# Kernel tuning notes

Hardware: AMD Instinct MI355X
Metric: run time of the kernel (lower is better)

Reference implementation:

```python
import jax, jax.numpy as jnp
import numpy as np

N_NODES = 10000
N_EDGES = 80000
N_GRAPHS = 64
HEADS = 8
F_IN = 128
D1, D2, D3 = 512, 256, 128  # per-head (and output, concat=False) widths
OUT_DIM = 10


def _lin(key, fin, fout):
    kw, kb = jax.random.split(key)
    w = jax.random.normal(kw, (fin, fout), dtype=jnp.float32) * 0.05
    b = jax.random.normal(kb, (fout,), dtype=jnp.float32) * 0.05
    return w, b


def setup_inputs() -> dict:
    key = jax.random.key(0)
    ks = jax.random.split(key, 24)
    x = jax.random.normal(ks[0], (N_NODES, F_IN), dtype=jnp.float32)
    edge_index = jax.random.randint(ks[1], (2, N_EDGES), 0, N_NODES, dtype=jnp.int64)
    batch = jnp.sort(jax.random.randint(ks[2], (N_NODES,), 0, N_GRAPHS, dtype=jnp.int64))
    d = {"x": x, "edge_index": edge_index, "batch": batch}
    # conv1: 128 -> heads*512 (q,k,v), skip 128 -> 512
    d["w_q1"], d["b_q1"] = _lin(ks[3], F_IN, HEADS * D1)
    d["w_k1"], d["b_k1"] = _lin(ks[4], F_IN, HEADS * D1)
    d["w_v1"], d["b_v1"] = _lin(ks[5], F_IN, HEADS * D1)
    d["w_s1"], d["b_s1"] = _lin(ks[6], F_IN, D1)
    # conv2: 512 -> heads*256, skip 512 -> 256
    d["w_q2"], d["b_q2"] = _lin(ks[7], D1, HEADS * D2)
    d["w_k2"], d["b_k2"] = _lin(ks[8], D1, HEADS * D2)
    d["w_v2"], d["b_v2"] = _lin(ks[9], D1, HEADS * D2)
    d["w_s2"], d["b_s2"] = _lin(ks[10], D1, D2)
    # conv3: 256 -> heads*128, skip 256 -> 128
    d["w_q3"], d["b_q3"] = _lin(ks[11], D2, HEADS * D3)
    d["w_k3"], d["b_k3"] = _lin(ks[12], D2, HEADS * D3)
    d["w_v3"], d["b_v3"] = _lin(ks[13], D2, HEADS * D3)
    d["w_s3"], d["b_s3"] = _lin(ks[14], D2, D3)
    # global attention gate + final fc
    d["w_g"], d["b_g"] = _lin(ks[15], D3, 1)
    d["w_fc"], d["b_fc"] = _lin(ks[16], D3, OUT_DIM)
    return d


def _seg_softmax(a, seg, n):
    m = jax.ops.segment_max(a, seg, num_segments=n)
    e = jnp.exp(a - m[seg])
    s = jax.ops.segment_sum(e, seg, num_segments=n)
    return e / (s[seg] + 1e-16)


def _tconv(x, edge_index, wq, bq, wk, bk, wv, bv, ws, bs):
    # PyG TransformerConv, concat=False, root_weight=True, no edge features
    n = x.shape[0]
    c = wq.shape[1] // HEADS
    q = (x @ wq + bq).reshape(n, HEADS, c)
    k = (x @ wk + bk).reshape(n, HEADS, c)
    v = (x @ wv + bv).reshape(n, HEADS, c)
    src, dst = edge_index[0], edge_index[1]
    a = jnp.einsum('ehc,ehc->eh', q[dst], k[src]) / jnp.sqrt(jnp.float32(c))
    alpha = _seg_softmax(a, dst, n)                                  # [E, H]
    out = jax.ops.segment_sum(v[src] * alpha[..., None], dst, num_segments=n)
    return out.mean(axis=1) + (x @ ws + bs)                          # mean over heads + skip


def reference(x, edge_index, batch,
              w_q1, b_q1, w_k1, b_k1, w_v1, b_v1, w_s1, b_s1,
              w_q2, b_q2, w_k2, b_k2, w_v2, b_v2, w_s2, b_s2,
              w_q3, b_q3, w_k3, b_k3, w_v3, b_v3, w_s3, b_s3,
              w_g, b_g, w_fc, b_fc):
    h = jax.nn.elu(_tconv(x, edge_index, w_q1, b_q1, w_k1, b_k1, w_v1, b_v1, w_s1, b_s1))
    h = jax.nn.elu(_tconv(h, edge_index, w_q2, b_q2, w_k2, b_k2, w_v2, b_v2, w_s2, b_s2))
    h = jax.nn.elu(_tconv(h, edge_index, w_q3, b_q3, w_k3, b_k3, w_v3, b_v3, w_s3, b_s3))
    # GlobalAttention pooling: softmax(gate) over nodes within each graph
    gate = h @ w_g + b_g                                             # [N, 1]
    gate = _seg_softmax(gate, batch, N_GRAPHS)
    g = jax.ops.segment_sum(gate * h, batch, num_segments=N_GRAPHS)  # [G, D3]
    return g @ w_fc + b_fc                                           # [G, OUT_DIM]
```

## Files before the change

kernel.cpp:

```cpp
#include <hip/hip_runtime.h>
#include <math.h>

typedef __bf16 bf16;
typedef __bf16 bf16x8 __attribute__((ext_vector_type(8)));
typedef __bf16 bf16x4 __attribute__((ext_vector_type(4)));
typedef __bf16 bf16x2 __attribute__((ext_vector_type(2)));
typedef float f32x4 __attribute__((ext_vector_type(4)));
typedef float f32x2 __attribute__((ext_vector_type(2)));
typedef unsigned int u32;

#define N_NODES 10000
#define N_EDGES 80000
#define N_GRAPHS 64

template<int EPL> struct VecT;
template<> struct VecT<8>{ typedef bf16x8 type; };
template<> struct VecT<4>{ typedef bf16x4 type; };
template<> struct VecT<2>{ typedef bf16x2 type; };

__device__ inline void gload_lds16(const bf16* g, bf16* l){
  __builtin_amdgcn_global_load_lds(
      (const __attribute__((address_space(1))) unsigned int*)g,
      (__attribute__((address_space(3))) unsigned int*)l, 16, 0, 0);
}

__global__ __launch_bounds__(256) void detect_f32_k(const unsigned short* __restrict__ raw, int n,
                                                    int* __restrict__ flagF){
  int i = blockIdx.x*256 + threadIdx.x;
  if (i < n){
    unsigned e = (raw[i] >> 7) & 0xFFu;
    if (e >= 0xC0u) atomicOr(flagF, 1);
  }
}

struct CvPack {
  const void* src[11];
  bf16* dst[11];
  int pre[12];
  int rl[11];
  int st[11];
};
__global__ __launch_bounds__(256) void convert_all(CvPack p, const int* __restrict__ flagF){
  int gid = blockIdx.x*256 + threadIdx.x;
  if (gid >= p.pre[11]) return;
  int t = 0;
  while (gid >= p.pre[t+1]) ++t;
  int i = gid - p.pre[t];
  bool f = (*flagF != 0);
  float v = f ? ((const float*)p.src[t])[i] : (float)((const bf16*)p.src[t])[i];
  int row = i / p.rl[t], col = i - row*p.rl[t];
  p.dst[t][(size_t)row*p.st[t] + col] = (bf16)v;
}

__global__ __launch_bounds__(256) void detect_i64(const int* __restrict__ raw, int* __restrict__ flag){
  int i = blockIdx.x*256 + threadIdx.x;
  if (i < 4000 && raw[2*i+1] != 0) atomicOr(flag, 1);
}

__global__ __launch_bounds__(256) void conv_idx(const int* __restrict__ ei_raw,
                                                const int* __restrict__ b_raw,
                                                const int* __restrict__ flag,
                                                int* __restrict__ src, int* __restrict__ dst,
                                                int* __restrict__ bat, int* __restrict__ cnt){
  int i = blockIdx.x*256 + threadIdx.x;
  bool i32 = (*flag != 0);
  if (i < N_EDGES){
    int s = i32 ? ei_raw[i]   : ei_raw[2*i];
    int d = i32 ? ei_raw[N_EDGES + i] : ei_raw[2*(N_EDGES + i)];
    s = min(max(s, 0), N_NODES-1);
    d = min(max(d, 0), N_NODES-1);
    src[i] = s; dst[i] = d;
    atomicAdd(&cnt[d], 1);
  }
  if (i < N_NODES){
    int b = i32 ? b_raw[i] : b_raw[2*i];
    bat[i] = min(max(b, 0), N_GRAPHS-1);
  }
}

__global__ __launch_bounds__(256) void scanA(const int* __restrict__ cnt, int* __restrict__ fill,
                                             int* __restrict__ bsum, int N){
  __shared__ int s[256];
  int i = blockIdx.x*256 + threadIdx.x;
  int v = (i < N) ? cnt[i] : 0;
  s[threadIdx.x] = v;
  __syncthreads();
  for (int d = 1; d < 256; d <<= 1){
    int t = (threadIdx.x >= d) ? s[threadIdx.x - d] : 0;
    __syncthreads();
    s[threadIdx.x] += t;
    __syncthreads();
  }
  if (i < N) fill[i] = s[threadIdx.x] - v;
  if (threadIdx.x == 255) bsum[blockIdx.x] = s[255];
}
__global__ __launch_bounds__(64) void scanB(int* __restrict__ bsum, int nb){
  if (threadIdx.x == 0){
    int a = 0;
    for (int b = 0; b < nb; ++b){ int t = bsum[b]; bsum[b] = a; a += t; }
  }
}
__global__ __launch_bounds__(256) void scanC(const int* __restrict__ bsum, int* __restrict__ fill,
                                             int* __restrict__ row_ptr, int N){
  int i = blockIdx.x*256 + threadIdx.x;
  if (i < N){
    int st = fill[i] + bsum[i >> 8];
    fill[i] = st;
    row_ptr[i] = st;
  }
  if (i == 0) row_ptr[N] = N_EDGES;
}

__global__ __launch_bounds__(256) void fill_csr(const int* __restrict__ dst,
                                                int* __restrict__ fill, int* __restrict__ eids){
  int e = blockIdx.x*256 + threadIdx.x;
  if (e < N_EDGES){
    int p = atomicAdd(&fill[dst[e]], 1);
    eids[p] = e;
  }
}

__global__ __launch_bounds__(256)
void gemm_bias(const bf16* __restrict__ A, int lda,
               const bf16* __restrict__ Bt,
               const bf16* __restrict__ bias, bf16* __restrict__ Cout, int ldc,
               int M, int N, int K)
{
  __shared__ bf16 As[128*64];
  __shared__ bf16 Bs[128*64];
  const int tid = threadIdx.x;
  const int lane = tid & 63;
  const int wave = tid >> 6;
  const int m0 = blockIdx.y * 128, n0 = blockIdx.x * 128;
  const int wm = (wave >> 1) * 64, wn = (wave & 1) * 64;
  const int l15 = lane & 15, l4 = lane >> 4;
  const int srow = lane >> 3;
  const int schunk = lane & 7;

  f32x4 acc[4][4] = {};

  for (int k0 = 0; k0 < K; k0 += 64){
    #pragma unroll
    for (int j = 0; j < 4; ++j){
      int r0 = (wave*4 + j)*8;
      int r  = r0 + srow;
      int gc = schunk ^ (r & 7);
      int ga = m0 + r; if (ga >= M) ga = M-1;
      gload_lds16(A  + (size_t)ga*lda      + k0 + gc*8, As + r0*64);
      gload_lds16(Bt + (size_t)(n0 + r)*K  + k0 + gc*8, Bs + r0*64);
    }
    __syncthreads();
    #pragma unroll
    for (int kt = 0; kt < 2; ++kt){
      bf16x8 af[4], bfr[4];
      #pragma unroll
      for (int mt = 0; mt < 4; ++mt){
        int row = wm + mt*16 + l15;
        int p = (kt*4 + l4) ^ (l15 & 7);
        af[mt] = *(const bf16x8*)(As + row*64 + p*8);
      }
      #pragma unroll
      for (int nt = 0; nt < 4; ++nt){
        int row = wn + nt*16 + l15;
        int p = (kt*4 + l4) ^ (l15 & 7);
        bfr[nt] = *(const bf16x8*)(Bs + row*64 + p*8);
      }
      #pragma unroll
      for (int mt = 0; mt < 4; ++mt)
        #pragma unroll
        for (int nt = 0; nt < 4; ++nt)
          acc[mt][nt] = __builtin_amdgcn_mfma_f32_16x16x32_bf16(af[mt], bfr[nt], acc[mt][nt], 0, 0, 0);
    }
    __syncthreads();
  }

  #pragma unroll
  for (int nt = 0; nt < 4; ++nt){
    int col = n0 + wn + nt*16 + l15;
    float bv = (float)bias[col];
    #pragma unroll
    for (int mt = 0; mt < 4; ++mt){
      int rbase = m0 + wm + mt*16 + l4*4;
      #pragma unroll
      for (int r = 0; r < 4; ++r){
        int row = rbase + r;
        if (row < M) Cout[(size_t)row*ldc + col] = (bf16)(acc[mt][nt][r] + bv);
      }
    }
  }
}

template<int NKB>
__global__ __launch_bounds__(512, 1)
void gemm_bres_bias(const bf16* __restrict__ A, int lda,
                    const bf16* __restrict__ Bt,
                    const bf16* __restrict__ bias, bf16* __restrict__ Cout, int ldc,
                    int M, int YB)
{
  constexpr int K = NKB*64;
  __shared__ bf16 Bs[NKB][128*64];
  const int tid = threadIdx.x;
  const int lane = tid & 63;
  const int wave = tid >> 6;
  const int n0 = blockIdx.x * 128;
  const int l15 = lane & 15, l4 = lane >> 4;
  const int srow = lane >> 3;
  const int schunk = lane & 7;

  #pragma unroll
  for (int kb = 0; kb < NKB; ++kb){
    #pragma unroll
    for (int j = 0; j < 2; ++j){
      int r0 = (wave*2 + j)*8;
      int r  = r0 + srow;
      int gc = schunk ^ srow;
      gload_lds16(Bt + (size_t)(n0 + r)*K + kb*64 + gc*8, &Bs[kb][r0*64]);
    }
  }
  asm volatile("s_waitcnt vmcnt(0)" ::: "memory");
  __builtin_amdgcn_s_barrier();

  float bv[8];
  #pragma unroll
  for (int nt = 0; nt < 8; ++nt) bv[nt] = (float)bias[n0 + nt*16 + l15];

  const int nstrips = (M + 63) >> 6;
  const int ws0 = blockIdx.y*8 + wave;
  const int wstep = YB*8;

  for (int strip = ws0; strip < nstrips; strip += wstep){
    const int m0 = strip*64;
    f32x4 acc[4][8] = {};
    #pragma unroll 2
    for (int kk = 0; kk < K/32; ++kk){
      const int kb = kk >> 1, kt = kk & 1;
      bf16x8 af[4];
      #pragma unroll
      for (int mt = 0; mt < 4; ++mt){
        int row = m0 + mt*16 + l15; if (row >= M) row = M-1;
        af[mt] = *(const bf16x8*)(A + (size_t)row*lda + kk*32 + l4*8);
      }
      bf16x8 bfr[8];
      #pragma unroll
      for (int nt = 0; nt < 8; ++nt){
        int p = (kt*4 + l4) ^ (l15 & 7);
        bfr[nt] = *(const bf16x8*)(&Bs[kb][(nt*16 + l15)*64 + p*8]);
      }
      #pragma unroll
      for (int mt = 0; mt < 4; ++mt)
        #pragma unroll
        for (int nt = 0; nt < 8; ++nt)
          acc[mt][nt] = __builtin_amdgcn_mfma_f32_16x16x32_bf16(af[mt], bfr[nt], acc[mt][nt], 0, 0, 0);
    }
    #pragma unroll
    for (int mt = 0; mt < 4; ++mt){
      int rbase = m0 + mt*16 + l4*4;
      #pragma unroll
      for (int r = 0; r < 4; ++r){
        int row = rbase + r;
        if (row < M){
          #pragma unroll
          for (int nt = 0; nt < 8; ++nt)
            Cout[(size_t)row*ldc + n0 + nt*16 + l15] = (bf16)(acc[mt][nt][r] + bv[nt]);
        }
      }
    }
  }
}

__global__ __launch_bounds__(512, 1)
void gemm8p_bias(const bf16* __restrict__ A, int lda,
                 const bf16* __restrict__ Bt,
                 const bf16* __restrict__ bias, bf16* __restrict__ Cout, int ldc,
                 int M, int K)
{
  __shared__ bf16 As[3][256*64];
  __shared__ bf16 Bs[3][128*64];
  const int tid = threadIdx.x;
  const int lane = tid & 63;
  const int wave = tid >> 6;
  const int m0 = blockIdx.y * 256, n0 = blockIdx.x * 128;
  const int wm = (wave >> 1) * 64;
  const int wn = (wave & 1) * 64;
  const int l15 = lane & 15, l4 = lane >> 4;
  const int srow = lane >> 3;
  const int schunk = lane & 7;
  const int NT = K >> 6;

  auto stageA = [&](int t, int j){
    int b = t % 3;
    int r0 = (wave + j*8)*8;
    int r  = r0 + srow;
    int gc = schunk ^ srow;
    int ga = m0 + r; if (ga >= M) ga = M-1;
    gload_lds16(A + (size_t)ga*lda + t*64 + gc*8, &As[b][r0*64]);
  };
  auto stageB = [&](int t, int j){
    int b = t % 3;
    int r0 = (wave + j*8)*8;
    int r  = r0 + srow;
    int gc = schunk ^ srow;
    gload_lds16(Bt + (size_t)(n0 + r)*K + t*64 + gc*8, &Bs[b][r0*64]);
  };

  stageA(0,0); stageA(0,1); stageA(0,2); stageA(0,3); stageB(0,0); stageB(0,1);
  if (NT > 1){ stageA(1,0); stageA(1,1); stageA(1,2); stageA(1,3); stageB(1,0); stageB(1,1); }
  if (NT > 1) asm volatile("s_waitcnt vmcnt(6)" ::: "memory");
  else        asm volatile("s_waitcnt vmcnt(0)" ::: "memory");
  __builtin_amdgcn_s_barrier();

  f32x4 acc[4][4] = {};

  for (int t = 0; t < NT; ++t){
    const bf16* as = &As[t % 3][0];
    const bf16* bs = &Bs[t % 3][0];
    bf16x8 bfr[4][2];
    bf16x8 af[2][2];

    #pragma unroll
    for (int nt2 = 0; nt2 < 4; ++nt2)
      #pragma unroll
      for (int kt = 0; kt < 2; ++kt){
        int row = wn + nt2*16 + l15;
        int p = (kt*4 + l4) ^ (l15 & 7);
        bfr[nt2][kt] = *(const bf16x8*)(bs + row*64 + p*8);
      }
    #pragma unroll
    for (int i = 0; i < 2; ++i)
      #pragma unroll
      for (int kt = 0; kt < 2; ++kt){
        int row = wm + i*16 + l15;
        int p = (kt*4 + l4) ^ (l15 & 7);
        af[i][kt] = *(const bf16x8*)(as + row*64 + p*8);
      }
    if (t + 2 < NT){ stageA(t+2,0); stageA(t+2,1); stageB(t+2,0); }
    __builtin_amdgcn_s_setprio(1);
    #pragma unroll
    for (int i = 0; i < 2; ++i)
      #pragma unroll
      for (int nt2 = 0; nt2 < 4; ++nt2)
        #pragma unroll
        for (int kt = 0; kt < 2; ++kt)
          acc[i][nt2] = __builtin_amdgcn_mfma_f32_16x16x32_bf16(af[i][kt], bfr[nt2][kt], acc[i][nt2], 0, 0, 0);
    __builtin_amdgcn_s_setprio(0);

    #pragma unroll
    for (int i = 0; i < 2; ++i)
      #pragma unroll
      for (int kt = 0; kt < 2; ++kt){
        int row = wm + (2+i)*16 + l15;
        int p = (kt*4 + l4) ^ (l15 & 7);
        af[i][kt] = *(const bf16x8*)(as + row*64 + p*8);
      }
    if (t + 2 < NT){ stageA(t+2,2); stageA(t+2,3); stageB(t+2,1); }
    __builtin_amdgcn_s_setprio(1);
    #pragma unroll
    for (int i = 0; i < 2; ++i)
      #pragma unroll
      for (int nt2 = 0; nt2 < 4; ++nt2)
        #pragma unroll
        for (int kt = 0; kt < 2; ++kt)
          acc[2+i][nt2] = __builtin_amdgcn_mfma_f32_16x16x32_bf16(af[i][kt], bfr[nt2][kt], acc[2+i][nt2], 0, 0, 0);
    __builtin_amdgcn_s_setprio(0);

    if (t < NT - 1){
      if (t + 2 < NT) asm volatile("s_waitcnt vmcnt(6)" ::: "memory");
      else            asm volatile("s_waitcnt vmcnt(0)" ::: "memory");
      __builtin_amdgcn_s_barrier();
    }
  }

  #pragma unroll
  for (int nt2 = 0; nt2 < 4; ++nt2){
    int col = n0 + wn + nt2*16 + l15;
    float bv = (float)bias[col];
    #pragma unroll
    for (int mt = 0; mt < 4; ++mt){
      int rbase = m0 + wm + mt*16 + l4*4;
      #pragma unroll
      for (int r = 0; r < 4; ++r){
        int row = rbase + r;
        if (row < M) Cout[(size_t)row*ldc + col] = (bf16)(acc[mt][nt2][r] + bv);
      }
    }
  }
}

template<int BM, int OUTMODE>
__global__ __launch_bounds__(256)
void gemm_fused(const bf16* __restrict__ A, int lda,
                const bf16* __restrict__ Bt,
                const bf16* __restrict__ bp, const bf16* __restrict__ mb,
                const int* __restrict__ row_ptr,
                bf16* __restrict__ outB, int ldo, float* __restrict__ outF,
                int M, int K)
{
  constexpr int PA    = BM/32;
  constexpr int WCOLS = 128/BM;
  constexpr int WTN   = BM;
  constexpr int NT    = WTN/16;
  __shared__ bf16 As[BM*64];
  __shared__ bf16 Bs[128*64];
  const int tid = threadIdx.x;
  const int lane = tid & 63;
  const int wave = tid >> 6;
  const int m0 = blockIdx.y * BM, n0 = blockIdx.x * 128;
  const int wm = (wave / WCOLS) * 32;
  const int wn = (wave % WCOLS) * WTN;
  const int l15 = lane & 15, l4 = lane >> 4;
  const int srow = lane >> 3;
  const int schunk = lane & 7;

  f32x4 acc[2][NT] = {};

  for (int k0 = 0; k0 < K; k0 += 64){
    #pragma unroll
    for (int j = 0; j < PA; ++j){
      int r0 = (wave*PA + j)*8;
      int r  = r0 + srow;
      int gc = schunk ^ (r & 7);
      int ga = m0 + r; if (ga >= M) ga = M-1;
      gload_lds16(A + (size_t)ga*lda + k0 + gc*8, As + r0*64);
    }
    #pragma unroll
    for (int j = 0; j < 4; ++j){
      int r0 = (wave*4 + j)*8;
      int r  = r0 + srow;
      int gc = schunk ^ (r & 7);
      gload_lds16(Bt + (size_t)(n0 + r)*K + k0 + gc*8, Bs + r0*64);
    }
    __syncthreads();
    #pragma unroll
    for (int kt = 0; kt < 2; ++kt){
      bf16x8 af[2], bfr[NT];
      #pragma unroll
      for (int mt = 0; mt < 2; ++mt){
        int row = wm + mt*16 + l15;
        int p = (kt*4 + l4) ^ (l15 & 7);
        af[mt] = *(const bf16x8*)(As + row*64 + p*8);
      }
      #pragma unroll
      for (int nt = 0; nt < NT; ++nt){
        int row = wn + nt*16 + l15;
        int p = (kt*4 + l4) ^ (l15 & 7);
        bfr[nt] = *(const bf16x8*)(Bs + row*64 + p*8);
      }
      #pragma unroll
      for (int mt = 0; mt < 2; ++mt)
        #pragma unroll
        for (int nt = 0; nt < NT; ++nt)
          acc[mt][nt] = __builtin_amdgcn_mfma_f32_16x16x32_bf16(af[mt], bfr[nt], acc[mt][nt], 0, 0, 0);
    }
    __syncthreads();
  }

  if (OUTMODE == 0){
    float bv[NT], mv[NT];
    #pragma unroll
    for (int nt = 0; nt < NT; ++nt){
      int col = n0 + wn + nt*16 + l15;
      bv[nt] = (float)bp[col];
      mv[nt] = (float)mb[col];
    }
    #pragma unroll
    for (int mt = 0; mt < 2; ++mt){
      int rbase = m0 + wm + mt*16 + l4*4;
      #pragma unroll
      for (int r = 0; r < 4; ++r){
        int row = rbase + r;
        if (row < M){
          bool d0 = (row_ptr[row+1] == row_ptr[row]);
          #pragma unroll
          for (int nt = 0; nt < NT; ++nt){
            int col = n0 + wn + nt*16 + l15;
            float v = acc[mt][nt][r] + bv[nt] - (d0 ? mv[nt] : 0.f);
            v = (v > 0.f) ? v : (__expf(v) - 1.f);
            outB[(size_t)row*ldo + col] = (bf16)v;
          }
        }
      }
    }
  } else {
    #pragma unroll
    for (int mt = 0; mt < 2; ++mt){
      int rbase = m0 + wm + mt*16 + l4*4;
      #pragma unroll
      for (int r = 0; r < 4; ++r){
        int row = rbase + r;
        if (row < M){
          #pragma unroll
          for (int nt = 0; nt < NT; ++nt){
            int col = n0 + wn + nt*16 + l15;
            outF[(size_t)row*128 + col] = acc[mt][nt][r];
          }
        }
      }
    }
  }
}

__global__ __launch_bounds__(256)
void finalize_gate(const float* __restrict__ facc, const bf16* __restrict__ bp,
                   const bf16* __restrict__ mb, const int* __restrict__ row_ptr,
                   bf16* __restrict__ hout, const bf16* __restrict__ wg,
                   const bf16* __restrict__ bg, float* __restrict__ gate)
{
  __shared__ float wred[4];
  int idx = blockIdx.x*256 + threadIdx.x;
  int n = idx >> 7, c = idx & 127;
  bool d0 = (row_ptr[n+1] == row_ptr[n]);
  float v = facc[idx] + (float)bp[c] - (d0 ? (float)mb[c] : 0.f);
  v = (v > 0.f) ? v : (__expf(v) - 1.f);
  hout[idx] = (bf16)v;
  float gc = v * (float)wg[c];
  #pragma unroll
  for (int o = 32; o; o >>= 1) gc += __shfl_xor(gc, o, 64);
  int wave = threadIdx.x >> 6;
  if ((threadIdx.x & 63) == 0) wred[wave] = gc;
  __syncthreads();
  if ((threadIdx.x & 127) == 0){
    float g = wred[wave] + wred[wave + 1] + (float)bg[0];
    gate[n] = g;
  }
}

__global__ __launch_bounds__(256)
void pool_graphs(const float* __restrict__ gate, const int* __restrict__ bat,
                 const bf16* __restrict__ h, float* __restrict__ gacc)
{
  int b = blockIdx.x;
  int lo = 0, hi = N_NODES;
  while (lo < hi){ int mid = (lo + hi) >> 1; if (bat[mid] < b) lo = mid + 1; else hi = mid; }
  int s = lo;
  lo = s; hi = N_NODES;
  while (lo < hi){ int mid = (lo + hi) >> 1; if (bat[mid] < b + 1) lo = mid + 1; else hi = mid; }
  int e = lo;

  int t = threadIdx.x;
  float m = -3.4e38f;
  for (int n = s + t; n < e; n += 256) m = fmaxf(m, gate[n]);
  #pragma unroll
  for (int o = 32; o; o >>= 1) m = fmaxf(m, __shfl_xor(m, o, 64));
  __shared__ float red[4];
  int wv = t >> 6;
  if ((t & 63) == 0) red[wv] = m;
  __syncthreads();
  m = fmaxf(fmaxf(red[0], red[1]), fmaxf(red[2], red[3]));

  int team = t >> 7, c = t & 127;
  float acc = 0.f, se = 0.f;
  for (int n = s + team; n < e; n += 2){
    float en = __expf(gate[n] - m);
    acc += en * (float)h[(size_t)n*128 + c];
    if (c == 0) se += en;
  }
  __shared__ float accs[256];
  __shared__ float ses[2];
  accs[t] = acc;
  if (c == 0) ses[team] = se;
  __syncthreads();
  if (t < 128){
    float tot = accs[t] + accs[128 + t];
    float S = ses[0] + ses[1];
    gacc[b*128 + t] = tot / (S + 1e-16f);
  }
}

struct MhPack { const bf16* wk[3]; const bf16* wq[3]; bf16* wzt[3]; int fin[3]; int c[3]; };
__global__ __launch_bounds__(256)
void gemm_mh_all(MhPack P)
{
  const int L = blockIdx.z >> 3, h = blockIdx.z & 7;
  const int Fin = P.fin[L], C = P.c[L];
  const int nb = Fin >> 7;
  if ((int)blockIdx.x >= nb || (int)blockIdx.y >= nb) return;
  __shared__ bf16 As[128*64];
  __shared__ bf16 Bs[128*64];
  const int ld = 8*C;
  const bf16* Ab = P.wk[L] + h*C;
  const bf16* Bb = P.wq[L] + h*C;
  bf16* Cb = P.wzt[L] + (size_t)h*Fin*Fin;
  const int tid = threadIdx.x;
  const int lane = tid & 63;
  const int wave = tid >> 6;
  const int m0 = blockIdx.y * 128, n0 = blockIdx.x * 128;
  const int wm = (wave >> 1) * 64, wn = (wave & 1) * 64;
  const int l15 = lane & 15, l4 = lane >> 4;
  const int srow = lane >> 3;
  const int schunk = lane & 7;

  f32x4 acc[4][4] = {};

  for (int k0 = 0; k0 < C; k0 += 64){
    #pragma unroll
    for (int j = 0; j < 4; ++j){
      int r0 = (wave*4 + j)*8;
      int r  = r0 + srow;
      int gc = schunk ^ (r & 7);
      gload_lds16(Ab + (size_t)(m0 + r)*ld + k0 + gc*8, As + r0*64);
      gload_lds16(Bb + (size_t)(n0 + r)*ld + k0 + gc*8, Bs + r0*64);
    }
    __syncthreads();
    #pragma unroll
    for (int kt = 0; kt < 2; ++kt){
      bf16x8 af[4], bfr[4];
      #pragma unroll
      for (int mt = 0; mt < 4; ++mt){
        int row = wm + mt*16 + l15;
        int p = (kt*4 + l4) ^ (l15 & 7);
        af[mt] = *(const bf16x8*)(As + row*64 + p*8);
      }
      #pragma unroll
      for (int nt = 0; nt < 4; ++nt){
        int row = wn + nt*16 + l15;
        int p = (kt*4 + l4) ^ (l15 & 7);
        bfr[nt] = *(const bf16x8*)(Bs + row*64 + p*8);
      }
      #pragma unroll
      for (int mt = 0; mt < 4; ++mt)
        #pragma unroll
        for (int nt = 0; nt < 4; ++nt)
          acc[mt][nt] = __builtin_amdgcn_mfma_f32_16x16x32_bf16(af[mt], bfr[nt], acc[mt][nt], 0, 0, 0);
    }
    __syncthreads();
  }

  #pragma unroll
  for (int nt = 0; nt < 4; ++nt){
    int col = n0 + wn + nt*16 + l15;
    #pragma unroll
    for (int mt = 0; mt < 4; ++mt){
      int rbase = m0 + wm + mt*16 + l4*4;
      #pragma unroll
      for (int r = 0; r < 4; ++r)
        Cb[(size_t)(rbase + r)*Fin + col] = (bf16)acc[mt][nt][r];
    }
  }
}

struct WvPack { const void* wv[3]; const void* ws[3]; bf16* bt[3]; int fin[3]; int c[3]; int bx[3]; int by[3]; };
__global__ __launch_bounds__(256)
void prep_wv_all(WvPack P, const int* __restrict__ flagF)
{
  const int L = blockIdx.z;
  if ((int)blockIdx.x >= P.bx[L] || (int)blockIdx.y >= P.by[L]) return;
  __shared__ float t[32][33];
  bool f = (*flagF != 0);
  const int Fin = P.fin[L], C = P.c[L];
  int k0 = blockIdx.x*32, j0 = blockIdx.y*32;
  int x = threadIdx.x & 31, y = threadIdx.x >> 5;
  const void* srcp; int nstride, cb; float sc; int i0;
  if (k0 < 8*Fin){
    int h = k0 / Fin; i0 = k0 - h*Fin;
    srcp = P.wv[L]; nstride = 8*C; cb = h*C + j0; sc = 0.125f;
  } else {
    i0 = k0 - 8*Fin;
    srcp = P.ws[L]; nstride = C; cb = j0; sc = 1.0f;
  }
  #pragma unroll
  for (int ii = 0; ii < 4; ++ii){
    int i = i0 + y + ii*8;
    size_t idx = (size_t)i*nstride + cb + x;
    float v = f ? ((const float*)srcp)[idx] : (float)((const bf16*)srcp)[idx];
    t[y + ii*8][x] = v*sc;
  }
  __syncthreads();
  #pragma unroll
  for (int ii = 0; ii < 4; ++ii){
    int j = j0 + y + ii*8;
    P.bt[L][(size_t)j*(9*Fin) + k0 + x] = (bf16)t[x][y + ii*8];
  }
}

struct SmPack { const bf16* wkc[3]; const void* bq[3]; const void* bv[3]; const void* bs[3];
                int fin[3]; int c[3]; bf16* tz[3]; bf16* bp[3]; bf16* mb[3]; int rb[3]; int bpb[3]; };
__global__ __launch_bounds__(256)
void prep_small_all(SmPack P, const int* __restrict__ flagF)
{
  const int L = blockIdx.z;
  const int Fin = P.fin[L], C = P.c[L];
  const int rb = P.rb[L];
  if ((int)blockIdx.x >= rb + P.bpb[L]) return;
  bool f = (*flagF != 0);
  if ((int)blockIdx.x < rb){
    int wave = threadIdx.x >> 6, lane = threadIdx.x & 63;
    int r = blockIdx.x*4 + wave;
    int h = r / Fin, i = r - h*Fin;
    int epc = C >> 6;
    const bf16* wp = P.wkc[L] + (size_t)i*8*C + h*C;
    const void* bqp = P.bq[L];
    float s = 0.f;
    for (int k = 0; k < epc; ++k){
      int c = k*64 + lane;
      float b = f ? ((const float*)bqp)[h*C + c] : (float)((const bf16*)bqp)[h*C + c];
      s += (float)wp[c] * b;
    }
    #pragma unroll
    for (int o = 32; o; o >>= 1) s += __shfl_xor(s, o, 64);
    if (lane == 0) P.tz[L][r] = (bf16)s;
  } else {
    int idx = ((int)blockIdx.x - rb)*256 + threadIdx.x;
    if (idx < C){
      float s = 0.f;
      for (int h = 0; h < 8; ++h)
        s += f ? ((const float*)P.bv[L])[h*C + idx] : (float)((const bf16*)P.bv[L])[h*C + idx];
      s *= 0.125f;
      float bsv = f ? ((const float*)P.bs[L])[idx] : (float)((const bf16*)P.bs[L])[idx];
      P.mb[L][idx] = (bf16)s;
      P.bp[L][idx] = (bf16)(s + bsv);
    }
  }
}

template<int Fin, int NHT>
__global__ __launch_bounds__(256)
void node_edge(const bf16* __restrict__ z, int zw, int hbase,
               bf16* __restrict__ AP, int ldP,
               const int* __restrict__ row_ptr, const int* __restrict__ eids,
               const int* __restrict__ srcv, float scale)
{
  constexpr int EPL  = Fin/64;
  constexpr int EPL2 = EPL/2;
  constexpr int KC   = Fin/32;
  typedef typename VecT<EPL>::type vecb;
  __shared__ float sw[4][68][12];

  const int wave = threadIdx.x >> 6;
  const int lane = threadIdx.x & 63;
  const int n = blockIdx.x*4 + wave;

  const int beg = row_ptr[n];
  int deg = row_ptr[n+1] - beg;
  if (deg > 64) deg = 64;

  bf16* APn = AP + (size_t)n*ldP;

  if (deg == 0){
    vecb zv;
    #pragma unroll
    for (int k = 0; k < EPL; ++k) zv[k] = (bf16)0.f;
    #pragma unroll
    for (int h = 0; h < NHT; ++h)
      *(vecb*)(APn + (size_t)(hbase + h)*Fin + lane*EPL) = zv;
    return;
  }

  int e_ld = (lane < deg) ? lane : 0;
  int srcReg = srcv[eids[beg + e_ld]];

  const int nc = (deg + 15) >> 4;
  const int l15 = lane & 15, l4 = lane >> 4;
  const int h   = l15 & (NHT-1);
  const bf16* zp = z + (size_t)n*zw + (size_t)h*Fin + l4*8;

  f32x4 sacc[4];
  #pragma unroll
  for (int c = 0; c < 4; ++c) sacc[c] = (f32x4){0.f,0.f,0.f,0.f};

  #pragma unroll
  for (int c = 0; c < 4; ++c){
    if (c < nc){
      int sn = __shfl(srcReg, c*16 + l15, 64);
      const bf16* ap = AP + (size_t)sn*ldP + 8*Fin + l4*8;
      f32x4 s = (f32x4){0.f,0.f,0.f,0.f};
      #pragma unroll
      for (int k = 0; k < KC; ++k){
        bf16x8 af = *(const bf16x8*)(ap + k*32);
        bf16x8 bv = *(const bf16x8*)(zp + k*32);
        s = __builtin_amdgcn_mfma_f32_16x16x32_bf16(af, bv, s, 0, 0, 0);
      }
      sacc[c] = s;
    }
  }

  float m = -3.4e38f;
  #pragma unroll
  for (int c = 0; c < 4; ++c){
    if (c < nc){
      #pragma unroll
      for (int r = 0; r < 4; ++r){
        int row = c*16 + l4*4 + r;
        float v = sacc[c][r]*scale;
        sacc[c][r] = v;
        if (row < deg) m = fmaxf(m, v);
      }
    }
  }
  m = fmaxf(m, __shfl_xor(m, 16, 64));
  m = fmaxf(m, __shfl_xor(m, 32, 64));
  float ssum = 0.f;
  #pragma unroll
  for (int c = 0; c < 4; ++c){
    if (c < nc){
      #pragma unroll
      for (int r = 0; r < 4; ++r){
        int row = c*16 + l4*4 + r;
        float e = (row < deg) ? __expf(sacc[c][r] - m) : 0.f;
        sacc[c][r] = e;
        ssum += e;
      }
    }
  }
  ssum += __shfl_xor(ssum, 16, 64);
  ssum += __shfl_xor(ssum, 32, 64);
  float inv = 1.f/(ssum + 1e-16f);

  if (l15 < NHT){
    #pragma unroll
    for (int c = 0; c < 4; ++c){
      if (c < nc){
        #pragma unroll
        for (int r = 0; r < 4; ++r)
          sw[wave][c*16 + l4*4 + r][l15] = sacc[c][r]*inv;
      }
    }
  }
  if (lane < 4*NHT)
    sw[wave][nc*16 + (lane >> 3)][lane & 7] = 0.f;

  f32x2 acc[NHT][EPL2];
  #pragma unroll
  for (int hh = 0; hh < NHT; ++hh)
    #pragma unroll
    for (int p = 0; p < EPL2; ++p) acc[hh][p] = (f32x2){0.f,0.f};

  for (int i0 = 0; i0 < deg; i0 += 4){
    int sn0 = __shfl(srcReg, i0,   64);
    int sn1 = __shfl(srcReg, i0+1, 64);
    int sn2 = __shfl(srcReg, i0+2, 64);
    int sn3 = __shfl(srcReg, i0+3, 64);
    vecb hv0 = *(const vecb*)(AP + (size_t)sn0*ldP + 8*Fin + lane*EPL);
    vecb hv1 = *(const vecb*)(AP + (size_t)sn1*ldP + 8*Fin + lane*EPL);
    vecb hv2 = *(const vecb*)(AP + (size_t)sn2*ldP + 8*Fin + lane*EPL);
    vecb hv3 = *(const vecb*)(AP + (size_t)sn3*ldP + 8*Fin + lane*EPL);
    #pragma unroll
    for (int j = 0; j < 4; ++j){
      int e = i0 + j;
      vecb hv = (j == 0) ? hv0 : (j == 1) ? hv1 : (j == 2) ? hv2 : hv3;
      f32x4 w0 = *(const f32x4*)&sw[wave][e][0];
      f32x4 w1 = (NHT == 8) ? *(const f32x4*)&sw[wave][e][4] : w0;
      f32x2 xf[EPL2];
      const u32* up = (const u32*)&hv;
      #pragma unroll
      for (int p = 0; p < EPL2; ++p){
        u32 u = up[p];
        xf[p] = (f32x2){ __uint_as_float(u << 16), __uint_as_float(u & 0xffff0000u) };
      }
      #pragma unroll
      for (int hh = 0; hh < NHT; ++hh){
        float w = (hh < 4) ? w0[hh] : w1[hh-4];
        f32x2 wv = (f32x2){w, w};
        #pragma unroll
        for (int p = 0; p < EPL2; ++p)
          acc[hh][p] += wv * xf[p];
      }
    }
  }

  #pragma unroll
  for (int hh = 0; hh < NHT; ++hh){
    vecb o;
    #pragma unroll
    for (int p = 0; p < EPL2; ++p){
      o[2*p]   = (bf16)acc[hh][p][0];
      o[2*p+1] = (bf16)acc[hh][p][1];
    }
    *(vecb*)(APn + (size_t)(hbase + hh)*Fin + lane*EPL) = o;
  }
}

__global__ __launch_bounds__(64) void final_fc(const float* __restrict__ gacc, const bf16* __restrict__ wfc,
                                               const bf16* __restrict__ bfc, void* __restrict__ out,
                                               const int* __restrict__ flagF){
  int g = blockIdx.x;
  int o = threadIdx.x;
  if (o < 10){
    float s = (float)bfc[o];
    for (int c = 0; c < 128; ++c) s += gacc[g*128 + c]*(float)wfc[c*10 + o];
    if (*flagF) ((float*)out)[(size_t)g*10 + o] = s;
    else        ((bf16*)out)[(size_t)g*10 + o]  = (bf16)s;
  }
}

extern "C" void kernel_launch(void* const* d_in, const int* in_sizes, int n_in,
                              void* d_out, int out_size, void* d_ws, size_t ws_size,
                              hipStream_t stream)
{
  const int* ei   = (const int*)d_in[1];
  const int* braw = (const int*)d_in[2];

  bf16 *Wzt1=0,*Wzt2=0,*Wzt3=0,*Wvt1=0,*Wvt2=0,*Wvt3=0;
  float *facc=0,*gate=0;
  bf16 *tz1=0,*tz2=0,*tz3=0,*bp1=0,*mb1=0,*bp2=0,*mb2=0,*bp3=0,*mb3=0,*h3=0;
  bf16 *cwg=0,*cbg=0,*cwfc=0,*cbfc=0;
  int *src=0,*dst=0,*bat=0,*cnt=0,*row_ptr=0,*fillp=0,*eids=0,*flagbuf=0;
  char *A1=0, *A2=0;

  auto plan = [&](bool big)->size_t{
    size_t off = 0;
    auto A = [&](size_t bytes)->char*{
      char* p = (char*)d_ws + off;
      off += (bytes + 255) & ~(size_t)255;
      return p;
    };
    A1 = A(92160000);
    A2 = A(big ? 81920000 : 46080000);
    Wzt1 = (bf16*)A((size_t)8*128*128*2);
    Wzt2 = (bf16*)A((size_t)8*512*512*2);
    Wzt3 = (bf16*)A((size_t)8*256*256*2);
    Wvt1 = (bf16*)A((size_t)512*9*128*2);
    Wvt2 = (bf16*)A((size_t)256*9*512*2);
    Wvt3 = (bf16*)A((size_t)128*9*256*2);
    facc = (float*)A((size_t)N_NODES*512*4);
    tz1  = (bf16*)A(8*128*2);
    tz2  = (bf16*)A(8*512*2);
    tz3  = (bf16*)A(8*256*2);
    bp1  = (bf16*)A(512*2);  mb1 = (bf16*)A(512*2);
    bp2  = (bf16*)A(256*2);  mb2 = (bf16*)A(256*2);
    bp3  = (bf16*)A(128*2);  mb3 = (bf16*)A(128*2);
    h3   = (bf16*)A((size_t)N_NODES*128*2);
    src  = (int*)A((size_t)N_EDGES*4);
    dst  = (int*)A((size_t)N_EDGES*4);
    bat  = (int*)A((size_t)N_NODES*4);
    cnt  = (int*)A((size_t)N_NODES*4);
    row_ptr = (int*)A((size_t)(N_NODES+1)*4);
    fillp= (int*)A((size_t)N_NODES*4);
    eids = (int*)A((size_t)N_EDGES*4);
    flagbuf = (int*)A(16384);
    gate = (float*)A((size_t)N_NODES*4);
    unsigned* poolz = (unsigned*)A((size_t)(64 + 64 + 64*128)*4);
    (void)poolz;
    cwg  = (bf16*)A(128*2);
    cbg  = (bf16*)A(2*2);
    cwfc = (bf16*)A(1280*2);
    cbfc = (bf16*)A(10*2);
    return off;
  };

  bool big = (plan(true) <= ws_size);
  if (!big && plan(false) > ws_size) return;
  plan(big);
  unsigned* poolz = (unsigned*)((char*)gate + (((size_t)N_NODES*4 + 255) & ~(size_t)255));

  int* flagI = flagbuf;
  int* flagF = flagbuf + 1;
  int* bsum  = (int*)((char*)flagbuf + 8192);
  float*    gacc = (float*)(poolz + 128);

  bf16* AP1 = (bf16*)A2;   const int ldP1 = 1152;
  bf16* z1  = (bf16*)A1;
  bf16* AP2 = (bf16*)A1;   const int ldP2 = 4608;
  bf16* z2  = (bf16*)A2;
  bf16* AP3 = (bf16*)A2;   const int ldP3 = 2304;
  bf16* z3  = (bf16*)A1;
  bf16* wq1c = (bf16*)(A1 + 48000000);  bf16* wk1c = wq1c + 128*4096;
  bf16* wq2c = wk1c + 128*4096;         bf16* wk2c = wq2c + 512*2048;
  bf16* wq3c = wk2c + 512*2048;         bf16* wk3c = wq3c + 256*1024;

  hipMemsetAsync(flagbuf, 0, 16384, stream);
  {
    int nprobe = in_sizes[0] < 32768 ? in_sizes[0] : 32768;
    detect_f32_k<<<(nprobe + 255)/256, 256, 0, stream>>>((const unsigned short*)d_in[0], nprobe, flagF);
    detect_i64<<<16, 256, 0, stream>>>(ei, flagI);
  }

  {
    CvPack p;
    const int CIDX[11] = {0, 3, 5, 11, 13, 19, 21, 27, 28, 29, 30};
    bf16* CDST[11] = {AP1 + 1024, wq1c, wk1c, wq2c, wk2c, wq3c, wk3c, cwg, cbg, cwfc, cbfc};
    int tot = 0;
    for (int t = 0; t < 11; ++t){
      p.src[t] = d_in[CIDX[t]];
      p.dst[t] = CDST[t];
      p.pre[t] = tot;
      int n = in_sizes[CIDX[t]];
      tot += n;
      if (t == 0){ p.rl[t] = 128; p.st[t] = 1152; }
      else       { p.rl[t] = n;   p.st[t] = n;    }
    }
    p.pre[11] = tot;
    convert_all<<<(tot + 255)/256, 256, 0, stream>>>(p, flagF);
  }

  hipMemsetAsync(cnt, 0, (size_t)N_NODES*4, stream);
  conv_idx<<<(N_EDGES + 255)/256, 256, 0, stream>>>(ei, braw, flagI, src, dst, bat, cnt);
  scanA<<<40, 256, 0, stream>>>(cnt, fillp, bsum, N_NODES);
  scanB<<<1, 64, 0, stream>>>(bsum, 40);
  scanC<<<40, 256, 0, stream>>>(bsum, fillp, row_ptr, N_NODES);
  fill_csr<<<(N_EDGES + 255)/256, 256, 0, stream>>>(dst, fillp, eids);

  {
    MhPack mp;
    mp.wk[0]=wk1c; mp.wk[1]=wk2c; mp.wk[2]=wk3c;
    mp.wq[0]=wq1c; mp.wq[1]=wq2c; mp.wq[2]=wq3c;
    mp.wzt[0]=Wzt1; mp.wzt[1]=Wzt2; mp.wzt[2]=Wzt3;
    mp.fin[0]=128; mp.fin[1]=512; mp.fin[2]=256;
    mp.c[0]=512; mp.c[1]=256; mp.c[2]=128;
    gemm_mh_all<<<dim3(4,4,24), 256, 0, stream>>>(mp);

    WvPack wp;
    wp.wv[0]=d_in[7];  wp.wv[1]=d_in[15]; wp.wv[2]=d_in[23];
    wp.ws[0]=d_in[9];  wp.ws[1]=d_in[17]; wp.ws[2]=d_in[25];
    wp.bt[0]=Wvt1; wp.bt[1]=Wvt2; wp.bt[2]=Wvt3;
    wp.fin[0]=128; wp.fin[1]=512; wp.fin[2]=256;
    wp.c[0]=512; wp.c[1]=256; wp.c[2]=128;
    wp.bx[0]=36; wp.bx[1]=144; wp.bx[2]=72;
    wp.by[0]=16; wp.by[1]=8;   wp.by[2]=4;
    prep_wv_all<<<dim3(144,16,3), 256, 0, stream>>>(wp, flagF);

    SmPack sp;
    sp.wkc[0]=wk1c; sp.wkc[1]=wk2c; sp.wkc[2]=wk3c;
    sp.bq[0]=d_in[4];  sp.bq[1]=d_in[12]; sp.bq[2]=d_in[20];
    sp.bv[0]=d_in[8];  sp.bv[1]=d_in[16]; sp.bv[2]=d_in[24];
    sp.bs[0]=d_in[10]; sp.bs[1]=d_in[18]; sp.bs[2]=d_in[26];
    sp.fin[0]=128; sp.fin[1]=512; sp.fin[2]=256;
    sp.c[0]=512; sp.c[1]=256; sp.c[2]=128;
    sp.tz[0]=tz1; sp.tz[1]=tz2; sp.tz[2]=tz3;
    sp.bp[0]=bp1; sp.bp[1]=bp2; sp.bp[2]=bp3;
    sp.mb[0]=mb1; sp.mb[1]=mb2; sp.mb[2]=mb3;
    sp.rb[0]=256;  sp.rb[1]=1024; sp.rb[2]=512;
    sp.bpb[0]=2;   sp.bpb[1]=1;   sp.bpb[2]=1;
    prep_small_all<<<dim3(1025,1,3), 256, 0, stream>>>(sp, flagF);
  }

  const int MT = (N_NODES + 127)/128;
  const int NB = N_NODES/4;
  const int MT32 = (N_NODES + 31)/32;
  const int MT64 = (N_NODES + 63)/64;
  const int MT256 = (N_NODES + 255)/256;
  const float sc1 = 1.0f/sqrtf(512.f), sc2 = 1.0f/sqrtf(256.f), sc3 = 1.0f/sqrtf(128.f);

  gemm_bias<<<dim3(8, MT), 256, 0, stream>>>(AP1 + 1024, ldP1, Wzt1, tz1, z1, 1024, N_NODES, 1024, 128);
  node_edge<128,8><<<NB, 256, 0, stream>>>(z1, 1024, 0, AP1, ldP1, row_ptr, eids, src, sc1);
  gemm_fused<64,0><<<dim3(4, MT64), 256, 0, stream>>>(AP1, ldP1, Wvt1, bp1, mb1, row_ptr,
                                                      AP2 + 4096, ldP2, (float*)0, N_NODES, 1152);

  if (big){
    gemm_bres_bias<8><<<dim3(32, 8), 512, 0, stream>>>(AP2 + 4096, ldP2, Wzt2, tz2, z2, 4096, N_NODES, 8);
    node_edge<512,8><<<NB, 256, 0, stream>>>(z2, 4096, 0, AP2, ldP2, row_ptr, eids, src, sc2);
  } else {
    for (int g = 0; g < 2; ++g){
      gemm_bias<<<dim3(16, MT), 256, 0, stream>>>(AP2 + 4096, ldP2, Wzt2 + (size_t)g*4*512*512, tz2 + g*4*512, z2, 2048, N_NODES, 2048, 512);
      node_edge<512,4><<<NB, 256, 0, stream>>>(z2, 2048, g*4, AP2, ldP2, row_ptr, eids, src, sc2);
    }
  }
  gemm_fused<32,0><<<dim3(2, MT32), 256, 0, stream>>>(AP2, ldP2, Wvt2, bp2, mb2, row_ptr,
                                                      AP3 + 2048, ldP3, (float*)0, N_NODES, 4608);

  gemm8p_bias<<<dim3(16, MT256), 512, 0, stream>>>(AP3 + 2048, ldP3, Wzt3, tz3, z3, 2048, N_NODES, 256);
  node_edge<256,8><<<NB, 256, 0, stream>>>(z3, 2048, 0, AP3, ldP3, row_ptr, eids, src, sc3);
  gemm_fused<32,1><<<dim3(1, MT32), 256, 0, stream>>>(AP3, ldP3, Wvt3, (const bf16*)0, (const bf16*)0, (const int*)0,
                                                      (bf16*)0, 0, facc, N_NODES, 2304);
  finalize_gate<<<(N_NODES*128)/256, 256, 0, stream>>>(facc, bp3, mb3, row_ptr, h3, cwg, cbg, gate);

  pool_graphs<<<N_GRAPHS, 256, 0, stream>>>(gate, bat, h3, gacc);
  final_fc<<<N_GRAPHS, 64, 0, stream>>>(gacc, cwfc, cbfc, d_out, flagF);
}
```

Measured before the change: 552.7 us.

## Replace B-resident strip GEMM with 2D-tiled LDS GEMM; widen conv2 fused tile

```diff
diff --git a/kernel.cpp b/kernel.cpp
--- a/kernel.cpp
+++ b/kernel.cpp
@@ -190,79 +190,73 @@
   }
 }
 
-template<int NKB>
-__global__ __launch_bounds__(512, 1)
-void gemm_bres_bias(const bf16* __restrict__ A, int lda,
-                    const bf16* __restrict__ Bt,
-                    const bf16* __restrict__ bias, bf16* __restrict__ Cout, int ldc,
-                    int M, int YB)
+__global__ __launch_bounds__(256, 4)
+void gemm_biasO(const bf16* __restrict__ A, int lda,
+                const bf16* __restrict__ Bt,
+                const bf16* __restrict__ bias, bf16* __restrict__ Cout, int ldc,
+                int M, int N, int K)
 {
-  constexpr int K = NKB*64;
-  __shared__ bf16 Bs[NKB][128*64];
+  __shared__ bf16 As[128*64];
+  __shared__ bf16 Bs[128*64];
   const int tid = threadIdx.x;
   const int lane = tid & 63;
   const int wave = tid >> 6;
-  const int n0 = blockIdx.x * 128;
+  const int m0 = blockIdx.y * 128, n0 = blockIdx.x * 128;
+  const int wm = (wave >> 1) * 64, wn = (wave & 1) * 64;
   const int l15 = lane & 15, l4 = lane >> 4;
   const int srow = lane >> 3;
   const int schunk = lane & 7;
 
-  #pragma unroll
-  for (int kb = 0; kb < NKB; ++kb){
-    #pragma unroll
-    for (int j = 0; j < 2; ++j){
-      int r0 = (wave*2 + j)*8;
+  f32x4 acc[4][4] = {};
+
+  for (int k0 = 0; k0 < K; k0 += 64){
+    #pragma unroll
+    for (int j = 0; j < 4; ++j){
+      int r0 = (wave*4 + j)*8;
       int r  = r0 + srow;
-      int gc = schunk ^ srow;
-      gload_lds16(Bt + (size_t)(n0 + r)*K + kb*64 + gc*8, &Bs[kb][r0*64]);
-    }
-  }
-  asm volatile("s_waitcnt vmcnt(0)" ::: "memory");
-  __builtin_amdgcn_s_barrier();
-
-  float bv[8];
-  #pragma unroll
-  for (int nt = 0; nt < 8; ++nt) bv[nt] = (float)bias[n0 + nt*16 + l15];
-
-  const int nstrips = (M + 63) >> 6;
-  const int ws0 = blockIdx.y*8 + wave;
-  const int wstep = YB*8;
-
-  for (int strip = ws0; strip < nstrips; strip += wstep){
-    const int m0 = strip*64;
-    f32x4 acc[4][8] = {};
-    #pragma unroll 2
-    for (int kk = 0; kk < K/32; ++kk){
-      const int kb = kk >> 1, kt = kk & 1;
-      bf16x8 af[4];
+      int gc = schunk ^ (r & 7);
+      int ga = m0 + r; if (ga >= M) ga = M-1;
+      gload_lds16(A  + (size_t)ga*lda      + k0 + gc*8, As + r0*64);
+      gload_lds16(Bt + (size_t)(n0 + r)*K  + k0 + gc*8, Bs + r0*64);
+    }
+    __syncthreads();
+    #pragma unroll
+    for (int kt = 0; kt < 2; ++kt){
+      bf16x8 af[4], bfr[4];
       #pragma unroll
       for (int mt = 0; mt < 4; ++mt){
-        int row = m0 + mt*16 + l15; if (row >= M) row = M-1;
-        af[mt] = *(const bf16x8*)(A + (size_t)row*lda + kk*32 + l4*8);
-      }
-      bf16x8 bfr[8];
-      #pragma unroll
-      for (int nt = 0; nt < 8; ++nt){
+        int row = wm + mt*16 + l15;
         int p = (kt*4 + l4) ^ (l15 & 7);
-        bfr[nt] = *(const bf16x8*)(&Bs[kb][(nt*16 + l15)*64 + p*8]);
+        af[mt] = *(const bf16x8*)(As + row*64 + p*8);
+      }
+      #pragma unroll
+      for (int nt = 0; nt < 4; ++nt){
+        int row = wn + nt*16 + l15;
+        int p = (kt*4 + l4) ^ (l15 & 7);
+        bfr[nt] = *(const bf16x8*)(Bs + row*64 + p*8);
       }
       #pragma unroll
       for (int mt = 0; mt < 4; ++mt)
         #pragma unroll
-        for (int nt = 0; nt < 8; ++nt)
+        for (int nt = 0; nt < 4; ++nt)
           acc[mt][nt] = __builtin_amdgcn_mfma_f32_16x16x32_bf16(af[mt], bfr[nt], acc[mt][nt], 0, 0, 0);
     }
-    #pragma unroll
-    for (int mt = 0; mt < 4; ++mt){
-      int rbase = m0 + mt*16 + l4*4;
-      #pragma unroll
-      for (int r = 0; r < 4; ++r){
-        int row = rbase + r;
-        if (row < M){
-          #pragma unroll
-          for (int nt = 0; nt < 8; ++nt)
-            Cout[(size_t)row*ldc + n0 + nt*16 + l15] = (bf16)(acc[mt][nt][r] + bv[nt]);
-        }
+    __syncthreads();
+  }
+
+  float bv[4];
+  #pragma unroll
+  for (int nt = 0; nt < 4; ++nt) bv[nt] = (float)bias[n0 + wn + nt*16 + l15];
+  #pragma unroll
+  for (int mt = 0; mt < 4; ++mt){
+    int rbase = m0 + wm + mt*16 + l4*4;
+    #pragma unroll
+    for (int r = 0; r < 4; ++r){
+      int row = rbase + r;
+      if (row < M){
+        #pragma unroll
+        for (int nt = 0; nt < 4; ++nt)
+          Cout[(size_t)row*ldc + n0 + wn + nt*16 + l15] = (bf16)(acc[mt][nt][r] + bv[nt]);
       }
     }
   }
@@ -1036,7 +1030,7 @@
                                                       AP2 + 4096, ldP2, (float*)0, N_NODES, 1152);
 
   if (big){
-    gemm_bres_bias<8><<<dim3(32, 8), 512, 0, stream>>>(AP2 + 4096, ldP2, Wzt2, tz2, z2, 4096, N_NODES, 8);
+    gemm_biasO<<<dim3(32, MT), 256, 0, stream>>>(AP2 + 4096, ldP2, Wzt2, tz2, z2, 4096, N_NODES, 4096, 512);
     node_edge<512,8><<<NB, 256, 0, stream>>>(z2, 4096, 0, AP2, ldP2, row_ptr, eids, src, sc2);
   } else {
     for (int g = 0; g < 2; ++g){
@@ -1044,7 +1038,7 @@
       node_edge<512,4><<<NB, 256, 0, stream>>>(z2, 2048, g*4, AP2, ldP2, row_ptr, eids, src, sc2);
     }
   }
-  gemm_fused<32,0><<<dim3(2, MT32), 256, 0, stream>>>(AP2, ldP2, Wvt2, bp2, mb2, row_ptr,
+  gemm_fused<64,0><<<dim3(2, MT64), 256, 0, stream>>>(AP2, ldP2, Wvt2, bp2, mb2, row_ptr,
                                                       AP3 + 2048, ldP3, (float*)0, N_NODES, 4608);
 
   gemm8p_bias<<<dim3(16, MT256), 512, 0, stream>>>(AP3 + 2048, ldP3, Wzt3, tz3, z3, 2048, N_NODES, 256);
```

After: 562.3 us. No clear change (+1.7%).
